# Performance work log

Hardware: AMD Instinct MI355X
Metric: run time of the kernel (lower is better)

The kernel has to match this reference:

```python
import jax, jax.numpy as jnp
import numpy as np

B, CIN, H, W = 8, 32, 64, 64  # x1/x2 each 32 ch; concat -> 64
C = 2 * CIN


def setup_inputs() -> dict:
    key = jax.random.key(0)
    ks = jax.random.split(key, 8)
    s = 0.05
    return {
        "x1": jax.random.normal(ks[0], (B, CIN, H, W), jnp.float32),
        "x2": jax.random.normal(ks[1], (B, CIN, H, W), jnp.float32),
        "Wq": jax.random.normal(ks[2], (C // 2, C), jnp.float32) * s,
        "bq": jax.random.normal(ks[3], (C // 2,), jnp.float32) * s,
        "Wk": jax.random.normal(ks[4], (C // 2, C), jnp.float32) * s,
        "bk": jax.random.normal(ks[5], (C // 2,), jnp.float32) * s,
        "Wv": jax.random.normal(ks[6], (C, C), jnp.float32) * s,
        "Wsc": jax.random.normal(ks[7], (C // 2, C), jnp.float32) * s,
        "gamma": jnp.array([0.5], jnp.float32),
    }


def reference(x1, x2, Wq, bq, Wk, bk, Wv, Wsc, gamma):
    x = jnp.concatenate([x1, x2], axis=1)  # [b, c, h, w]
    b, c, h, w = x.shape
    hw = h * w
    # 1x1 convs == per-pixel linear projections
    q = (jnp.einsum('oc,bchw->bohw', Wq, x) + bq[None, :, None, None]).reshape(b, c // 2, hw)
    q = q.transpose(0, 2, 1)  # [b, hw, c/2]
    k = (jnp.einsum('oc,bchw->bohw', Wk, x) + bk[None, :, None, None]).reshape(b, c // 2, hw)
    am = jnp.einsum('bnd,bdm->bnm', q, k)  # [b, hw, hw]
    a = jax.nn.softmax(am, axis=1)  # softmax over dim=1 (queries axis) as in the torch code
    v = jnp.einsum('oc,bchw->bohw', Wv, x).reshape(b, c, hw)  # [b, c, hw]
    # out = bmm(v, a^T): out[b,c,n] = sum_m v[b,c,m] * a[b,n,m]
    out = jnp.einsum('bcm,bnm->bcn', v, a).reshape(b, c, h, w)
    out = gamma[0] * out + x
    out = jnp.einsum('oc,bchw->bohw', Wsc, out)  # [b, c/2, h, w]
    return out
```

## Files before the change

kernel.cpp:

```cpp
#include <hip/hip_runtime.h>

typedef __attribute__((ext_vector_type(8))) __bf16 bf16x8;
typedef __attribute__((ext_vector_type(4))) float f32x4;
typedef _Float16 f16x4 __attribute__((ext_vector_type(4)));
typedef unsigned int uint32;

#define HW   4096
#define CCH  64
#define DQ   32
#define OC   32
#define LOG2E 1.4426950408889634f

#define WSV_OFF  0u
#define QB_OFF   2048u
#define KB_OFF   (QB_OFF + 524288u)
#define XS_OFF   (KB_OFF + 524288u)
#define V2_OFF   (XS_OFF + 1048576u)
#define ZP_OFF   (V2_OFF + 1048576u)
#define VZC_OFF  (ZP_OFF + 262144u)
#define OUTP_OFF (VZC_OFF + 524288u)

__device__ __forceinline__ uint32 f2bf(float x) {
    uint32 u = __builtin_bit_cast(uint32, x);
    return (u + 0x7fffu + ((u >> 16) & 1u)) >> 16;
}
__device__ __forceinline__ uint32 packbf(float a, float b) {
    return f2bf(a) | (f2bf(b) << 16);
}
__device__ __forceinline__ bf16x8 ldfrag(const unsigned short* p) {
    union { uint4 u; bf16x8 f; } t;
    t.u = *(const uint4*)p;
    return t.f;
}
__device__ __forceinline__ f16x4 u2h4(uint32 a, uint32 b) {
    union { uint2 u; f16x4 f; } t;
    t.u.x = a; t.u.y = b;
    return t.f;
}
__device__ __forceinline__ f16x4 pk4(float a, float b, float c, float d) {
    union { uint2 u; f16x4 f; } t;
    t.u.x = __builtin_bit_cast(uint32, __builtin_amdgcn_cvt_pkrtz(a, b));
    t.u.y = __builtin_bit_cast(uint32, __builtin_amdgcn_cvt_pkrtz(c, d));
    return t.f;
}
__device__ __forceinline__ float fexp2(float x) {
#if __has_builtin(__builtin_amdgcn_exp2f)
    return __builtin_amdgcn_exp2f(x);
#else
    return __expf(x * 0.6931471805599453f);
#endif
}

__global__ __launch_bounds__(256) void k_wcomb(const float* __restrict__ Wsc,
                                               const float* __restrict__ Wv,
                                               float* __restrict__ Wsv) {
    int t = blockIdx.x * 256 + threadIdx.x;
    if (t < OC * CCH) {
        int o = t / CCH, ci = t % CCH;
        float s = 0.f;
        #pragma unroll
        for (int c = 0; c < CCH; ++c) s += Wsc[o * CCH + c] * Wv[c * CCH + ci];
        Wsv[t] = s;
    }
}

__global__ __launch_bounds__(256) void k_proj(
    const float* __restrict__ x1, const float* __restrict__ x2,
    const float* __restrict__ Wq, const float* __restrict__ bq,
    const float* __restrict__ Wk, const float* __restrict__ bk,
    const float* __restrict__ Wsv, const float* __restrict__ Wsc,
    unsigned short* __restrict__ qb, unsigned short* __restrict__ kb,
    float* __restrict__ v2, float* __restrict__ xs) {
    int t = threadIdx.x;
    int g = __builtin_amdgcn_readfirstlane(t >> 6);
    int l = t & 63;
    int p = blockIdx.x * 64 + l;
    int b = p >> 12, n = p & 4095;
    const float* x1b = x1 + (size_t)b * 32 * HW + n;
    const float* x2b = x2 + (size_t)b * 32 * HW + n;
    float x[CCH];
    #pragma unroll
    for (int c = 0; c < 32; ++c) x[c] = x1b[(size_t)c * HW];
    #pragma unroll
    for (int c = 0; c < 32; ++c) x[32 + c] = x2b[(size_t)c * HW];

    if (g < 2) {
        const float* W    = g ? Wk : Wq;
        const float* bias = g ? bk : bq;
        float scale = g ? 1.0f : LOG2E;
        unsigned short* dst = g ? kb : qb;
        size_t row = ((size_t)b * HW + n) * DQ;
        for (int d0 = 0; d0 < DQ; d0 += 8) {
            float r[8];
            #pragma unroll
            for (int i = 0; i < 8; ++i) {
                const float* wr = W + (d0 + i) * CCH;
                float a = bias[d0 + i];
                #pragma unroll
                for (int c = 0; c < CCH; ++c) a += wr[c] * x[c];
                r[i] = a * scale;
            }
            uint4 u;
            u.x = packbf(r[0], r[1]); u.y = packbf(r[2], r[3]);
            u.z = packbf(r[4], r[5]); u.w = packbf(r[6], r[7]);
            *(uint4*)(dst + row + d0) = u;
        }
    } else {
        const float* W = (g == 2) ? Wsv : Wsc;
        float* dst     = (g == 2) ? v2  : xs;
        for (int o = 0; o < OC; ++o) {
            const float* wr = W + o * CCH;
            float a = 0.f;
            #pragma unroll
            for (int c = 0; c < CCH; ++c) a += wr[c] * x[c];
            dst[((size_t)b * OC + o) * HW + n] = a;
        }
    }
}

__global__ __launch_bounds__(128, 4) void k_stats(
    const unsigned short* __restrict__ kb, const unsigned short* __restrict__ qb,
    float* __restrict__ zp) {
    int t = threadIdx.x;
    int w = t >> 6, l = t & 63;
    int lr = l & 15, lq = l >> 4;
    int bid = blockIdx.x;
    int b = bid & 7, nc = (bid >> 3) & 7, mg = bid >> 6;
    int m0 = mg * 256 + w * 128;

    const unsigned short* kbb = kb + (size_t)b * HW * DQ;
    bf16x8 af[8];
    #pragma unroll
    for (int f = 0; f < 8; ++f)
        af[f] = ldfrag(kbb + (size_t)(m0 + f * 16 + lr) * DQ + lq * 8);

    const unsigned short* qp = qb + ((size_t)b * HW + nc * 512 + lr) * DQ + lq * 8;

    f32x4 acc[8];
    #pragma unroll
    for (int f = 0; f < 8; ++f) acc[f] = (f32x4){0.f, 0.f, 0.f, 0.f};
    f32x4 zz = {0.f, 0.f, 0.f, 0.f};

    for (int i = 0; i < 32; ++i) {
        bf16x8 qf = ldfrag(qp);
        qp += 16 * DQ;
        #pragma unroll
        for (int f = 0; f < 8; ++f) {
            f32x4 s = __builtin_amdgcn_mfma_f32_16x16x32_bf16(af[f], qf, zz, 0, 0, 0);
            acc[f].x += fexp2(s.x); acc[f].y += fexp2(s.y);
            acc[f].z += fexp2(s.z); acc[f].w += fexp2(s.w);
        }
    }
    #pragma unroll
    for (int f = 0; f < 8; ++f) {
        #pragma unroll
        for (int off = 1; off < 16; off <<= 1) {
            acc[f].x += __shfl_xor(acc[f].x, off);
            acc[f].y += __shfl_xor(acc[f].y, off);
            acc[f].z += __shfl_xor(acc[f].z, off);
            acc[f].w += __shfl_xor(acc[f].w, off);
        }
    }
    if (lr == 0) {
        size_t base = (size_t)nc * 32768 + (size_t)b * HW;
        #pragma unroll
        for (int f = 0; f < 8; ++f) {
            size_t p0 = base + m0 + f * 16 + lq * 4;
            zp[p0 + 0] = acc[f].x;
            zp[p0 + 1] = acc[f].y;
            zp[p0 + 2] = acc[f].z;
            zp[p0 + 3] = acc[f].w;
        }
    }
}

__global__ __launch_bounds__(256) void k_zvz(const float* __restrict__ zp,
                                             const float* __restrict__ v2,
                                             const float* __restrict__ gamma,
                                             unsigned short* __restrict__ vzc) {
    int i = blockIdx.x * 256 + threadIdx.x;
    float s = 0.f;
    #pragma unroll
    for (int nc = 0; nc < 8; ++nc) s += zp[nc * 32768 + i];
    float zs = gamma[0] / s;
    int b = i >> 12, m = i & 4095;
    int Mb = m >> 5, mloc = m & 31;
    int ph = mloc >> 4, lqm = (mloc >> 2) & 3, j = mloc & 3;
    const float* vsrc = v2 + ((size_t)b * OC) * HW + m;
    unsigned short* dst = vzc + (size_t)b * OC * HW + (size_t)Mb * 1024
                        + lqm * 8 + ph * 4 + j;
    #pragma unroll 8
    for (int o = 0; o < OC; ++o) {
        _Float16 h = (_Float16)(vsrc[(size_t)o * HW] * zs);
        dst[o * 32] = __builtin_bit_cast(unsigned short, h);
    }
}

__global__ __launch_bounds__(128, 2) void k_attn(
    const unsigned short* __restrict__ qb, const unsigned short* __restrict__ kb,
    const unsigned short* __restrict__ vzc, unsigned short* __restrict__ outp) {
    int t = threadIdx.x;
    int w = t >> 6, l = t & 63;
    int lr = l & 15, lq = l >> 4;
    int bid = blockIdx.x;
    int b = bid & 7, mc = (bid >> 3) & 7, ng = bid >> 6;
    int n0 = ng * 256 + w * 128;

    bf16x8 qf[8];
    #pragma unroll
    for (int tt = 0; tt < 8; ++tt)
        qf[tt] = ldfrag(qb + ((size_t)b * HW + n0 + tt * 16 + lr) * DQ + lq * 8);

    const unsigned short* kp = kb + ((size_t)b * HW + lr) * DQ + lq * 8;
    const unsigned short* vp = vzc + (size_t)b * OC * HW + lr * 32 + lq * 8;

    f32x4 acc0[8], acc1[8];
    #pragma unroll
    for (int tt = 0; tt < 8; ++tt) {
        acc0[tt] = (f32x4){0.f, 0.f, 0.f, 0.f};
        acc1[tt] = (f32x4){0.f, 0.f, 0.f, 0.f};
    }
    f32x4 zz = {0.f, 0.f, 0.f, 0.f};

    int mbeg = mc * 512;
    for (int m0 = mbeg; m0 < mbeg + 512; m0 += 32) {
        int Mb = m0 >> 5;
        uint4 vv0 = *(const uint4*)(vp + (size_t)Mb * 1024);
        uint4 vv1 = *(const uint4*)(vp + (size_t)Mb * 1024 + 512);
        #pragma unroll
        for (int ph = 0; ph < 2; ++ph) {
            int mb = m0 + ph * 16;
            bf16x8 a  = ldfrag(kp + (size_t)mb * DQ);
            f16x4 va0 = ph ? u2h4(vv0.z, vv0.w) : u2h4(vv0.x, vv0.y);
            f16x4 va1 = ph ? u2h4(vv1.z, vv1.w) : u2h4(vv1.x, vv1.y);
            #pragma unroll
            for (int tt = 0; tt < 8; ++tt) {
                f32x4 s = __builtin_amdgcn_mfma_f32_16x16x32_bf16(a, qf[tt], zz, 0, 0, 0);
                f16x4 p = pk4(fexp2(s.x), fexp2(s.y), fexp2(s.z), fexp2(s.w));
                acc0[tt] = __builtin_amdgcn_mfma_f32_16x16x16f16(va0, p, acc0[tt], 0, 0, 0);
                acc1[tt] = __builtin_amdgcn_mfma_f32_16x16x16f16(va1, p, acc1[tt], 0, 0, 0);
            }
        }
    }

    unsigned short* ob = outp + (size_t)(mc * 8 + b) * OC * HW;
    #pragma unroll
    for (int tt = 0; tt < 8; ++tt) {
        int n_t = n0 + tt * 16 + lr;
        #pragma unroll
        for (int r = 0; r < 4; ++r) {
            int o0 = lq * 4 + r;
            ob[(size_t)o0 * HW + n_t]        = (unsigned short)f2bf(acc0[tt][r]);
            ob[(size_t)(o0 + 16) * HW + n_t] = (unsigned short)f2bf(acc1[tt][r]);
        }
    }
}

__global__ __launch_bounds__(256) void k_red(const unsigned short* __restrict__ outp,
                                             const float* __restrict__ xs,
                                             float* __restrict__ out) {
    int i = (blockIdx.x * 256 + threadIdx.x) * 4;
    float4 r = *(const float4*)(xs + i);
    const unsigned short* op = outp + i;
    #pragma unroll
    for (int mc = 0; mc < 8; ++mc) {
        uint2 p = *(const uint2*)(op + (size_t)mc * 1048576);
        r.x += __builtin_bit_cast(float, p.x << 16);
        r.y += __builtin_bit_cast(float, p.x & 0xffff0000u);
        r.z += __builtin_bit_cast(float, p.y << 16);
        r.w += __builtin_bit_cast(float, p.y & 0xffff0000u);
    }
    *(float4*)(out + i) = r;
}

extern "C" void kernel_launch(void* const* d_in, const int* in_sizes, int n_in,
                              void* d_out, int out_size, void* d_ws, size_t ws_size,
                              hipStream_t stream) {
    const float* x1    = (const float*)d_in[0];
    const float* x2    = (const float*)d_in[1];
    const float* Wq    = (const float*)d_in[2];
    const float* bq    = (const float*)d_in[3];
    const float* Wk    = (const float*)d_in[4];
    const float* bk    = (const float*)d_in[5];
    const float* Wv    = (const float*)d_in[6];
    const float* Wsc   = (const float*)d_in[7];
    const float* gamma = (const float*)d_in[8];
    float* out = (float*)d_out;
    float* ws  = (float*)d_ws;

    float*          wsv  = ws + WSV_OFF;
    unsigned short* qbp  = (unsigned short*)(ws + QB_OFF);
    unsigned short* kbp  = (unsigned short*)(ws + KB_OFF);
    float*          xsp  = ws + XS_OFF;
    float*          v2   = ws + V2_OFF;
    float*          zpp  = ws + ZP_OFF;
    unsigned short* vzc  = (unsigned short*)(ws + VZC_OFF);
    unsigned short* outp = (unsigned short*)(ws + OUTP_OFF);

    k_wcomb<<<8, 256, 0, stream>>>(Wsc, Wv, wsv);
    k_proj<<<512, 256, 0, stream>>>(x1, x2, Wq, bq, Wk, bk, wsv, Wsc,
                                    qbp, kbp, v2, xsp);
    k_stats<<<1024, 128, 0, stream>>>(kbp, qbp, zpp);
    k_zvz<<<128, 256, 0, stream>>>(zpp, v2, gamma, vzc);
    k_attn<<<1024, 128, 0, stream>>>(qbp, kbp, vzc, outp);
    k_red<<<1024, 256, 0, stream>>>(outp, xsp, out);
}
```

Before: 167.1 us.

## Fold weight combine into projection and re-split attention into larger blocks

Removes the separate Wsc·Wv kernel and has every projection block recompute the combined weight into shared memory. The stats and attention kernels move from 128-thread blocks over 8 chunks to 256-thread blocks over 4 chunks of the key/query axis, which halves the partial sums written and reduced. Periodic __syncthreads are added to keep the waves of a block in lockstep for cache reuse of the shared K/Q stream. The zvz kernel is split across two threads per position. In exchange, 512 blocks each redo a small matmul, and the grids for stats and attention shrink to 256 blocks, which may underfill the device.

After: 214.1 us. +28.1%, slower.

```diff
diff --git a/kernel.cpp b/kernel.cpp
--- a/kernel.cpp
+++ b/kernel.cpp
@@ -11,13 +11,12 @@
 #define OC   32
 #define LOG2E 1.4426950408889634f
 
-#define WSV_OFF  0u
-#define QB_OFF   2048u
+#define QB_OFF   0u
 #define KB_OFF   (QB_OFF + 524288u)
 #define XS_OFF   (KB_OFF + 524288u)
 #define V2_OFF   (XS_OFF + 1048576u)
 #define ZP_OFF   (V2_OFF + 1048576u)
-#define VZC_OFF  (ZP_OFF + 262144u)
+#define VZC_OFF  (ZP_OFF + 131072u)
 #define OUTP_OFF (VZC_OFF + 524288u)
 
 __device__ __forceinline__ uint32 f2bf(float x) {
@@ -51,27 +50,26 @@
 #endif
 }
 
-__global__ __launch_bounds__(256) void k_wcomb(const float* __restrict__ Wsc,
-                                               const float* __restrict__ Wv,
-                                               float* __restrict__ Wsv) {
-    int t = blockIdx.x * 256 + threadIdx.x;
-    if (t < OC * CCH) {
-        int o = t / CCH, ci = t % CCH;
-        float s = 0.f;
-        #pragma unroll
-        for (int c = 0; c < CCH; ++c) s += Wsc[o * CCH + c] * Wv[c * CCH + ci];
-        Wsv[t] = s;
-    }
-}
-
 __global__ __launch_bounds__(256) void k_proj(
     const float* __restrict__ x1, const float* __restrict__ x2,
     const float* __restrict__ Wq, const float* __restrict__ bq,
     const float* __restrict__ Wk, const float* __restrict__ bk,
-    const float* __restrict__ Wsv, const float* __restrict__ Wsc,
+    const float* __restrict__ Wv, const float* __restrict__ Wsc,
     unsigned short* __restrict__ qb, unsigned short* __restrict__ kb,
     float* __restrict__ v2, float* __restrict__ xs) {
+    __shared__ float wsvL[OC * CCH];
     int t = threadIdx.x;
+    #pragma unroll
+    for (int i = 0; i < 8; ++i) {
+        int e = t * 8 + i;
+        int o = e >> 6, ci = e & 63;
+        float s = 0.f;
+        #pragma unroll
+        for (int c = 0; c < CCH; ++c) s += Wsc[o * CCH + c] * Wv[c * CCH + ci];
+        wsvL[e] = s;
+    }
+    __syncthreads();
+
     int g = __builtin_amdgcn_readfirstlane(t >> 6);
     int l = t & 63;
     int p = blockIdx.x * 64 + l;
@@ -105,28 +103,34 @@
             u.z = packbf(r[4], r[5]); u.w = packbf(r[6], r[7]);
             *(uint4*)(dst + row + d0) = u;
         }
-    } else {
-        const float* W = (g == 2) ? Wsv : Wsc;
-        float* dst     = (g == 2) ? v2  : xs;
+    } else if (g == 2) {
         for (int o = 0; o < OC; ++o) {
-            const float* wr = W + o * CCH;
+            const float* wr = wsvL + o * CCH;
             float a = 0.f;
             #pragma unroll
             for (int c = 0; c < CCH; ++c) a += wr[c] * x[c];
-            dst[((size_t)b * OC + o) * HW + n] = a;
-        }
-    }
-}
-
-__global__ __launch_bounds__(128, 4) void k_stats(
+            v2[((size_t)b * OC + o) * HW + n] = a;
+        }
+    } else {
+        for (int o = 0; o < OC; ++o) {
+            const float* wr = Wsc + o * CCH;
+            float a = 0.f;
+            #pragma unroll
+            for (int c = 0; c < CCH; ++c) a += wr[c] * x[c];
+            xs[((size_t)b * OC + o) * HW + n] = a;
+        }
+    }
+}
+
+__global__ __launch_bounds__(256, 2) void k_stats(
     const unsigned short* __restrict__ kb, const unsigned short* __restrict__ qb,
     float* __restrict__ zp) {
     int t = threadIdx.x;
     int w = t >> 6, l = t & 63;
     int lr = l & 15, lq = l >> 4;
     int bid = blockIdx.x;
-    int b = bid & 7, nc = (bid >> 3) & 7, mg = bid >> 6;
-    int m0 = mg * 256 + w * 128;
+    int b = bid & 7, nc = (bid >> 3) & 3, mg = bid >> 5;
+    int m0 = mg * 512 + w * 128;
 
     const unsigned short* kbb = kb + (size_t)b * HW * DQ;
     bf16x8 af[8];
@@ -134,14 +138,15 @@
     for (int f = 0; f < 8; ++f)
         af[f] = ldfrag(kbb + (size_t)(m0 + f * 16 + lr) * DQ + lq * 8);
 
-    const unsigned short* qp = qb + ((size_t)b * HW + nc * 512 + lr) * DQ + lq * 8;
+    const unsigned short* qp = qb + ((size_t)b * HW + nc * 1024 + lr) * DQ + lq * 8;
 
     f32x4 acc[8];
     #pragma unroll
     for (int f = 0; f < 8; ++f) acc[f] = (f32x4){0.f, 0.f, 0.f, 0.f};
     f32x4 zz = {0.f, 0.f, 0.f, 0.f};
 
-    for (int i = 0; i < 32; ++i) {
+    for (int i = 0; i < 64; ++i) {
+        if ((i & 7) == 0) __syncthreads();
         bf16x8 qf = ldfrag(qp);
         qp += 16 * DQ;
         #pragma unroll
@@ -178,33 +183,35 @@
                                              const float* __restrict__ v2,
                                              const float* __restrict__ gamma,
                                              unsigned short* __restrict__ vzc) {
-    int i = blockIdx.x * 256 + threadIdx.x;
+    int idx = blockIdx.x * 256 + threadIdx.x;
+    int i = idx >> 1, half = idx & 1;
     float s = 0.f;
     #pragma unroll
-    for (int nc = 0; nc < 8; ++nc) s += zp[nc * 32768 + i];
+    for (int nc = 0; nc < 4; ++nc) s += zp[nc * 32768 + i];
     float zs = gamma[0] / s;
     int b = i >> 12, m = i & 4095;
     int Mb = m >> 5, mloc = m & 31;
     int ph = mloc >> 4, lqm = (mloc >> 2) & 3, j = mloc & 3;
-    const float* vsrc = v2 + ((size_t)b * OC) * HW + m;
+    int o0 = half * 16;
+    const float* vsrc = v2 + ((size_t)b * OC + o0) * HW + m;
     unsigned short* dst = vzc + (size_t)b * OC * HW + (size_t)Mb * 1024
-                        + lqm * 8 + ph * 4 + j;
+                        + o0 * 32 + lqm * 8 + ph * 4 + j;
     #pragma unroll 8
-    for (int o = 0; o < OC; ++o) {
+    for (int o = 0; o < 16; ++o) {
         _Float16 h = (_Float16)(vsrc[(size_t)o * HW] * zs);
         dst[o * 32] = __builtin_bit_cast(unsigned short, h);
     }
 }
 
-__global__ __launch_bounds__(128, 2) void k_attn(
+__global__ __launch_bounds__(256, 2) void k_attn(
     const unsigned short* __restrict__ qb, const unsigned short* __restrict__ kb,
     const unsigned short* __restrict__ vzc, unsigned short* __restrict__ outp) {
     int t = threadIdx.x;
     int w = t >> 6, l = t & 63;
     int lr = l & 15, lq = l >> 4;
     int bid = blockIdx.x;
-    int b = bid & 7, mc = (bid >> 3) & 7, ng = bid >> 6;
-    int n0 = ng * 256 + w * 128;
+    int b = bid & 7, mc = (bid >> 3) & 3, ng = bid >> 5;
+    int n0 = ng * 512 + w * 128;
 
     bf16x8 qf[8];
     #pragma unroll
@@ -222,8 +229,9 @@
     }
     f32x4 zz = {0.f, 0.f, 0.f, 0.f};
 
-    int mbeg = mc * 512;
-    for (int m0 = mbeg; m0 < mbeg + 512; m0 += 32) {
+    int mbeg = mc * 1024;
+    for (int m0 = mbeg; m0 < mbeg + 1024; m0 += 32) {
+        if ((m0 & 127) == 0) __syncthreads();
         int Mb = m0 >> 5;
         uint4 vv0 = *(const uint4*)(vp + (size_t)Mb * 1024);
         uint4 vv1 = *(const uint4*)(vp + (size_t)Mb * 1024 + 512);
@@ -263,7 +271,7 @@
     float4 r = *(const float4*)(xs + i);
     const unsigned short* op = outp + i;
     #pragma unroll
-    for (int mc = 0; mc < 8; ++mc) {
+    for (int mc = 0; mc < 4; ++mc) {
         uint2 p = *(const uint2*)(op + (size_t)mc * 1048576);
         r.x += __builtin_bit_cast(float, p.x << 16);
         r.y += __builtin_bit_cast(float, p.x & 0xffff0000u);
@@ -288,7 +296,6 @@
     float* out = (float*)d_out;
     float* ws  = (float*)d_ws;
 
-    float*          wsv  = ws + WSV_OFF;
     unsigned short* qbp  = (unsigned short*)(ws + QB_OFF);
     unsigned short* kbp  = (unsigned short*)(ws + KB_OFF);
     float*          xsp  = ws + XS_OFF;
@@ -297,11 +304,10 @@
     unsigned short* vzc  = (unsigned short*)(ws + VZC_OFF);
     unsigned short* outp = (unsigned short*)(ws + OUTP_OFF);
 
-    k_wcomb<<<8, 256, 0, stream>>>(Wsc, Wv, wsv);
-    k_proj<<<512, 256, 0, stream>>>(x1, x2, Wq, bq, Wk, bk, wsv, Wsc,
+    k_proj<<<512, 256, 0, stream>>>(x1, x2, Wq, bq, Wk, bk, Wv, Wsc,
                                     qbp, kbp, v2, xsp);
-    k_stats<<<1024, 128, 0, stream>>>(kbp, qbp, zpp);
-    k_zvz<<<128, 256, 0, stream>>>(zpp, v2, gamma, vzc);
-    k_attn<<<1024, 128, 0, stream>>>(qbp, kbp, vzc, outp);
+    k_stats<<<256, 256, 0, stream>>>(kbp, qbp, zpp);
+    k_zvz<<<256, 256, 0, stream>>>(zpp, v2, gamma, vzc);
+    k_attn<<<256, 256, 0, stream>>>(qbp, kbp, vzc, outp);
     k_red<<<1024, 256, 0, stream>>>(outp, xsp, out);
 }
```
